# Performance work log

Measured on AMD Instinct MI355X. Metric: run time of the kernel, lower is better.

Reference implementation:

```python
import math
import jax, jax.numpy as jnp
import numpy as np

B, P, L, D = 2, 32, 32, 768
N = P * L
H = 12
HD = D // H
FF = 4 * D
NL = 12
NC = 1000
EPS = 1e-5
NEG = -jnp.finfo(jnp.float32).max


def sinusoidal_pe(P, L, D):
    pe = np.zeros((P, L, D), dtype=np.float32)
    half = D // 2
    div = np.exp(np.arange(0.0, half, 2) * -(math.log(10000.0) / half))  # (half/2,)
    pos_l = np.arange(0.0, L)[:, None]
    pos_n = np.arange(0.0, P)[:, None]
    # faithful to the (buggy) torch builder, which requires P == L
    pe[:, :, 0:half:2] = np.sin(pos_n * div)[None, :, :]
    pe[:, :, 1:half:2] = np.cos(pos_n * div)[None, :, :]
    pe[:, :, half::2] = np.sin(pos_l * div)[:, None, :]
    pe[:, :, half + 1::2] = np.cos(pos_l * div)[:, None, :]
    return pe.reshape(P * L, D)


def layernorm(x, w, b):
    mu = jnp.mean(x, axis=-1, keepdims=True)
    var = jnp.var(x, axis=-1, keepdims=True)
    return (x - mu) * jax.lax.rsqrt(var + EPS) * w + b


def setup_inputs() -> dict:
    key = jax.random.key(0)
    ks = jax.random.split(key, 16)
    tn = lambda k, shp: (0.02 * jax.random.normal(k, shp)).astype(jnp.float32)
    inp = {
        "x": jax.random.normal(ks[0], (B, N, D), dtype=jnp.float32),
        "mask": jax.random.randint(ks[1], (B, N), 0, 2).astype(bool),
        "pe": jnp.asarray(sinusoidal_pe(P, L, D)),
        "ln0_w": jnp.ones((NL, D)), "ln0_b": jnp.zeros((NL, D)),
        "qkv_w": tn(ks[2], (NL, D, 3 * D)),
        "proj_w": tn(ks[3], (NL, D, D)), "proj_b": jnp.zeros((NL, D)),
        "ln1_w": jnp.ones((NL, D)), "ln1_b": jnp.zeros((NL, D)),
        "ff1_w": tn(ks[4], (NL, D, FF)), "ff1_b": jnp.zeros((NL, FF)),
        "ff2_w": tn(ks[5], (NL, FF, D)), "ff2_b": jnp.zeros((NL, D)),
        "norm_w": jnp.ones((D,)), "norm_b": jnp.zeros((D,)),
        "pool_w": tn(ks[6], (D, 1)), "pool_b": jnp.zeros((1,)),
        "fc_w": tn(ks[7], (D, NC)), "fc_b": jnp.zeros((NC,)),
    }
    return inp


def reference(x, mask, pe, ln0_w, ln0_b, qkv_w, proj_w, proj_b, ln1_w, ln1_b,
              ff1_w, ff1_b, ff2_w, ff2_b, norm_w, norm_b, pool_w, pool_b, fc_w, fc_b):
    scale = HD ** -0.5
    mask2 = mask[:, None, :] & mask[:, :, None]  # (B,N,N)

    def blk(h, p):
        g0w, g0b, qw, pw, pb, g1w, g1b, f1w, f1b, f2w, f2b = p
        y = layernorm(h, g0w, g0b)
        qkv = (y @ qw).reshape(B, N, 3, H, HD).transpose(2, 0, 3, 1, 4)  # (3,B,H,N,hd)
        q, k, v = qkv[0], qkv[1], qkv[2]
        attn = jnp.einsum('bhnd,bhmd->bhnm', q, k) * scale
        attn = jnp.where(mask2[:, None, :, :], attn, NEG)
        attn = jax.nn.softmax(attn, axis=-1)
        o = jnp.einsum('bhnm,bhmd->bhnd', attn, v)
        o = o.transpose(0, 2, 1, 3).reshape(B, N, D) @ pw + pb
        h = layernorm(h + o, g1w, g1b)
        ff = jax.nn.gelu(h @ f1w + f1b, approximate=False) @ f2w + f2b
        return h + ff, None

    h = x + pe[None]
    params = (ln0_w, ln0_b, qkv_w, proj_w, proj_b, ln1_w, ln1_b, ff1_w, ff1_b, ff2_w, ff2_b)
    h, _ = jax.lax.scan(blk, h, params)
    h = layernorm(h, norm_w, norm_b)
    # seq-pool: softmax over tokens of a learned scalar score
    w = jax.nn.softmax(h @ pool_w + pool_b, axis=1)  # (B,N,1)
    pooled = jnp.einsum('bnc,bnd->bd', w, h)  # c == 1
    return pooled @ fc_w + fc_b
```

## Files before the change

kernel.cpp:

```cpp
#include <hip/hip_runtime.h>
#include <hip/hip_bf16.h>
#include <cfloat>
#include <cmath>

typedef __bf16 bf16x8 __attribute__((ext_vector_type(8)));
typedef __bf16 bf16x4 __attribute__((ext_vector_type(4)));
typedef float  f32x4  __attribute__((ext_vector_type(4)));

static constexpr int Bb = 2, Nn = 1024, Dd = 768, Hh = 12, HDd = 64, FFf = 3072, NLl = 12, NCc = 1000;
static constexpr int Mm = Bb * Nn;
static constexpr float NEGF = -3.402823466e38f;

__device__ __forceinline__ float block_reduce_sum(float v, volatile float* smem) {
  for (int o = 32; o; o >>= 1) v += __shfl_down(v, o);
  int lane = threadIdx.x & 63, w = threadIdx.x >> 6;
  __syncthreads();
  if (lane == 0) smem[w] = v;
  __syncthreads();
  return smem[0] + smem[1] + smem[2] + smem[3];
}

__device__ __forceinline__ float block_reduce_max(float v, volatile float* smem) {
  for (int o = 32; o; o >>= 1) v = fmaxf(v, __shfl_down(v, o));
  int lane = threadIdx.x & 63, w = threadIdx.x >> 6;
  __syncthreads();
  if (lane == 0) smem[w] = v;
  __syncthreads();
  return fmaxf(fmaxf(smem[0], smem[1]), fmaxf(smem[2], smem[3]));
}

__global__ void detect_mask(const unsigned char* __restrict__ m, int* __restrict__ flag) {
  __shared__ int s_nz1, s_nz2, s_nz3, s_nz84, s_pv;
  int tid = threadIdx.x;
  if (tid == 0) { s_nz1 = 0; s_nz2 = 0; s_nz3 = 0; s_nz84 = 0; s_pv = 0; }
  __syncthreads();
  int nz1 = 0, nz2 = 0, nz3 = 0, nz84 = 0, pv = 0;
  for (int i = tid; i < 2048; i += 256) {
    unsigned char v = m[i];
    if (v) {
      int p4 = i & 3;
      if (p4 == 1) nz1 = 1;
      if (p4 == 2) nz2 = 1;
      if (p4 == 3) nz3 = 1;
      if ((i & 7) == 4) nz84 = 1;
      if ((i & 1) == 0) { if (v != 0x80) pv = 1; }
      else              { if (v != 0x3f) pv = 1; }
    }
  }
  if (nz1)  atomicOr(&s_nz1, 1);
  if (nz2)  atomicOr(&s_nz2, 1);
  if (nz3)  atomicOr(&s_nz3, 1);
  if (nz84) atomicOr(&s_nz84, 1);
  if (pv)   atomicOr(&s_pv, 1);
  __syncthreads();
  if (tid == 0) {
    int f;
    if (!s_nz1 && !s_nz2 && !s_nz3) f = s_nz84 ? 0 : 3;
    else if (!s_pv)                 f = s_nz1 ? 4 : 2;
    else                            f = 1;
    *flag = f;
  }
}

__device__ __forceinline__ bool mask_at(const void* mraw, int flag, int idx) {
  switch (flag) {
    case 0:  return ((const int*)mraw)[idx] != 0;
    case 1:  return ((const unsigned char*)mraw)[idx] != 0;
    case 2:  return ((const float*)mraw)[idx] != 0.f;
    case 3:  return ((const long long*)mraw)[idx] != 0;
    default: return ((const unsigned short*)mraw)[idx] != 0;
  }
}

__device__ __forceinline__ void cvt8_store(const float* __restrict__ s, __bf16* __restrict__ d, int j) {
  float4 f0 = reinterpret_cast<const float4*>(s)[j * 2];
  float4 f1 = reinterpret_cast<const float4*>(s)[j * 2 + 1];
  bf16x8 r;
  r[0] = (__bf16)f0.x; r[1] = (__bf16)f0.y; r[2] = (__bf16)f0.z; r[3] = (__bf16)f0.w;
  r[4] = (__bf16)f1.x; r[5] = (__bf16)f1.y; r[6] = (__bf16)f1.z; r[7] = (__bf16)f1.w;
  reinterpret_cast<bf16x8*>(d)[j] = r;
}

__global__ __launch_bounds__(256) void cvt_w(const float* __restrict__ src, __bf16* __restrict__ dst, int n8) {
  int i = blockIdx.x * 256 + threadIdx.x;
  if (i < n8) cvt8_store(src, dst, i);
}

__global__ __launch_bounds__(256) void cvt_w4(const float* __restrict__ sq, const float* __restrict__ sp,
                                              const float* __restrict__ s1, const float* __restrict__ s2,
                                              __bf16* __restrict__ dq, __bf16* __restrict__ dp,
                                              __bf16* __restrict__ d1, __bf16* __restrict__ d2) {
  const int N0 = Dd * 3 * Dd / 8, N1 = Dd * Dd / 8, N2 = Dd * FFf / 8, N3 = FFf * Dd / 8;
  int i = blockIdx.x * 256 + threadIdx.x;
  if (i < N0)                    cvt8_store(sq, dq, i);
  else if (i < N0 + N1)          cvt8_store(sp, dp, i - N0);
  else if (i < N0 + N1 + N2)     cvt8_store(s1, d1, i - N0 - N1);
  else if (i < N0 + N1 + N2 + N3) cvt8_store(s2, d2, i - N0 - N1 - N2);
}

__global__ __launch_bounds__(256) void add_pe_k(const float* __restrict__ x, const float* __restrict__ pe,
                                                float* __restrict__ h) {
  long i = (long)blockIdx.x * 256 + threadIdx.x;
  long nd = i % ((long)Nn * Dd);
  h[i] = x[i] + pe[nd];
}

template<int OBF>
__global__ __launch_bounds__(256) void ln_kernel(const float* __restrict__ X,
                                                 const float* __restrict__ w, const float* __restrict__ b,
                                                 void* __restrict__ Y) {
  __shared__ float smem[4];
  int row = blockIdx.x, tid = threadIdx.x;
  const float* x = X + (size_t)row * Dd;
  float v[3];
  for (int j = 0; j < 3; ++j) v[j] = x[tid + j * 256];
  float s = v[0] + v[1] + v[2];
  s = block_reduce_sum(s, smem);
  float mean = s * (1.f / 768.f);
  float q = 0.f;
  for (int j = 0; j < 3; ++j) { float d = v[j] - mean; q += d * d; }
  q = block_reduce_sum(q, smem);
  float inv = rsqrtf(q * (1.f / 768.f) + 1e-5f);
  for (int j = 0; j < 3; ++j) {
    int c = tid + j * 256;
    float r = (v[j] - mean) * inv * w[c] + b[c];
    if (OBF) ((__bf16*)Y)[(size_t)row * Dd + c] = (__bf16)r;
    else     ((float*)Y)[(size_t)row * Dd + c] = r;
  }
}

template<int OBF, int HRES>
__global__ __launch_bounds__(256) void res_ln_kernel(float* __restrict__ H,
                                                     const float* __restrict__ P0, const float* __restrict__ P1,
                                                     const float* __restrict__ pb,
                                                     const float* __restrict__ w, const float* __restrict__ b,
                                                     void* __restrict__ Y) {
  __shared__ float smem[4];
  int row = blockIdx.x, tid = threadIdx.x;
  float* x  = H  + (size_t)row * Dd;
  const float* p0 = P0 + (size_t)row * Dd;
  const float* p1 = P1 + (size_t)row * Dd;
  float v[3];
  for (int j = 0; j < 3; ++j) {
    int c = tid + j * 256;
    v[j] = x[c] + (p0[c] + p1[c] + pb[c]);
  }
  float s = v[0] + v[1] + v[2];
  s = block_reduce_sum(s, smem);
  float mean = s * (1.f / 768.f);
  float q = 0.f;
  for (int j = 0; j < 3; ++j) { float d = v[j] - mean; q += d * d; }
  q = block_reduce_sum(q, smem);
  float inv = rsqrtf(q * (1.f / 768.f) + 1e-5f);
  for (int j = 0; j < 3; ++j) {
    int c = tid + j * 256;
    float r = (v[j] - mean) * inv * w[c] + b[c];
    x[c] = HRES ? v[j] : r;
    if (OBF) ((__bf16*)Y)[(size_t)row * Dd + c] = (__bf16)r;
    else     ((float*)Y)[(size_t)row * Dd + c] = r;
  }
}

template<int BN, int EPI, int OBF>
__global__ __launch_bounds__(256) void gemm128(
    const __bf16* __restrict__ Ap, long lda,
    const __bf16* __restrict__ Bp, long ldb,
    const float* __restrict__ bias,
    void* __restrict__ Cp, long ldc,
    int Ksize, long czs)
{
  constexpr int FN = BN / 32;
  constexpr int KB = BN / 8;
  int tid = threadIdx.x;

  int nwg2 = gridDim.x * gridDim.y;
  int bid = blockIdx.y * gridDim.x + blockIdx.x;
  int swz = (bid & 7) * (nwg2 >> 3) + (bid >> 3);
  int bx = swz % gridDim.x, by = swz / gridDim.x;
  int m0 = by * 128, n0 = bx * BN;
  int z = blockIdx.z;

  const __bf16* Aq = Ap + (long)z * Ksize;
  const __bf16* Bq = Bp + (long)z * Ksize * ldb;

  __shared__ __align__(16) __bf16 Ah[128][40];
  __shared__ __align__(16) __bf16 Bh[BN][40];

  f32x4 acc[4][FN];
  #pragma unroll
  for (int i = 0; i < 4; ++i)
    #pragma unroll
    for (int j = 0; j < FN; ++j)
      #pragma unroll
      for (int k = 0; k < 4; ++k) acc[i][j][k] = 0.f;

  int lane = tid & 63;
  int w = tid >> 6;
  int WR = (w >> 1) * 64, WC = (w & 1) * (BN / 2);
  int fr = lane & 15, kg = lane >> 4;

  const int ar = tid >> 1, acs = (tid & 1) * 16;
  const int bn = tid % BN;
  const int kb = (tid / BN) * KB;

  const __bf16* Abase = Aq + (long)(m0 + ar) * lda + acs;
  const __bf16* Bbase = Bq + (long)kb * ldb + (n0 + bn);

  bf16x8 pa0, pa1;
  __bf16 pbh[KB];
  {
    pa0 = *reinterpret_cast<const bf16x8*>(Abase);
    pa1 = *reinterpret_cast<const bf16x8*>(Abase + 8);
    #pragma unroll
    for (int j = 0; j < KB; ++j) pbh[j] = Bbase[(long)j * ldb];
  }

  for (int k0 = 0; k0 < Ksize; k0 += 32) {
    __syncthreads();
    {
      *reinterpret_cast<bf16x8*>(&Ah[ar][acs]) = pa0;
      *reinterpret_cast<bf16x8*>(&Ah[ar][acs + 8]) = pa1;
      #pragma unroll
      for (int g8 = 0; g8 < KB / 8; ++g8)
        *reinterpret_cast<bf16x8*>(&Bh[bn][kb + g8 * 8]) = *reinterpret_cast<bf16x8*>(&pbh[g8 * 8]);
    }
    __syncthreads();

    if (k0 + 32 < Ksize) {
      const __bf16* As = Abase + (k0 + 32);
      pa0 = *reinterpret_cast<const bf16x8*>(As);
      pa1 = *reinterpret_cast<const bf16x8*>(As + 8);
      const __bf16* Bs = Bbase + (long)(k0 + 32) * ldb;
      #pragma unroll
      for (int j = 0; j < KB; ++j) pbh[j] = Bs[(long)j * ldb];
    }

    bf16x8 ah[4], bh[FN];
    #pragma unroll
    for (int fm = 0; fm < 4; ++fm)
      ah[fm] = *reinterpret_cast<const bf16x8*>(&Ah[WR + fm * 16 + fr][kg * 8]);
    #pragma unroll
    for (int fn = 0; fn < FN; ++fn)
      bh[fn] = *reinterpret_cast<const bf16x8*>(&Bh[WC + fn * 16 + fr][kg * 8]);
    #pragma unroll
    for (int fm = 0; fm < 4; ++fm)
      #pragma unroll
      for (int fn = 0; fn < FN; ++fn)
        acc[fm][fn] = __builtin_amdgcn_mfma_f32_16x16x32_bf16(ah[fm], bh[fn], acc[fm][fn], 0, 0, 0);
  }

  #pragma unroll
  for (int fm = 0; fm < 4; ++fm)
    #pragma unroll
    for (int fn = 0; fn < FN; ++fn)
      #pragma unroll
      for (int i = 0; i < 4; ++i) {
        int rowg = m0 + WR + fm * 16 + kg * 4 + i;
        int coln = n0 + WC + fn * 16 + fr;
        float v = acc[fm][fn][i];
        if (EPI >= 1) v += bias[coln];
        if (EPI == 2) v = 0.5f * v * (1.f + erff(v * 0.70710678118654752f));
        long ci = (long)z * czs + (long)rowg * ldc + coln;
        if (OBF) ((__bf16*)Cp)[ci] = (__bf16)v;
        else     ((float*)Cp)[ci] = v;
      }
}

__global__ __launch_bounds__(256) void flash_attn_split(const __bf16* __restrict__ qkvb,
                                                        const void* __restrict__ mraw,
                                                        const int* __restrict__ flagp,
                                                        float* __restrict__ p0, float* __restrict__ p1,
                                                        float2* __restrict__ ml) {
  __shared__ __align__(16) __bf16 Qs[64][72];
  __shared__ __align__(16) __bf16 Ks[64][72];
  __shared__ __align__(16) __bf16 Vt[64][66];
  __shared__ __align__(16) __bf16 Ps[64][72];
  __shared__ float kmf[64];
  __shared__ float qmf[64];

  int s = blockIdx.z & 1, b = blockIdx.z >> 1;
  int hh = blockIdx.y;
  int q0 = blockIdx.x * 64;
  int tid = threadIdx.x, lane = tid & 63, w = tid >> 6;
  int flag = *flagp;
  int fr = lane & 15, kg = lane >> 4;

  const int sr = tid >> 2;
  const int sc = (tid & 3) * 16;

  {
    const __bf16* Qsrc = qkvb + ((long)(b * Nn + q0 + sr)) * (3 * Dd) + hh * HDd + sc;
    *reinterpret_cast<bf16x8*>(&Qs[sr][sc])     = *reinterpret_cast<const bf16x8*>(Qsrc);
    *reinterpret_cast<bf16x8*>(&Qs[sr][sc + 8]) = *reinterpret_cast<const bf16x8*>(Qsrc + 8);
    if (tid < 64) qmf[tid] = mask_at(mraw, flag, b * Nn + q0 + tid) ? 1.f : 0.f;
  }
  __syncthreads();

  float qm[4];
  #pragma unroll
  for (int i = 0; i < 4; ++i) qm[i] = qmf[16 * w + kg * 4 + i];

  bf16x8 qa[2];
  #pragma unroll
  for (int ks = 0; ks < 2; ++ks)
    qa[ks] = *reinterpret_cast<const bf16x8*>(&Qs[16 * w + fr][ks * 32 + kg * 8]);

  float mrow[4], lrow[4];
  f32x4 accO[4];
  #pragma unroll
  for (int i = 0; i < 4; ++i) { mrow[i] = -INFINITY; lrow[i] = 0.f; }
  #pragma unroll
  for (int t = 0; t < 4; ++t)
    for (int i = 0; i < 4; ++i) accO[t][i] = 0.f;

  const int jbeg = s * (Nn / 2), jend = jbeg + (Nn / 2);

  bf16x8 rk0, rk1, rv0, rv1;
  {
    const __bf16* Ksrc = qkvb + ((long)(b * Nn + jbeg + sr)) * (3 * Dd) + Dd + hh * HDd + sc;
    const __bf16* Vsrc = Ksrc + Dd;
    rk0 = *reinterpret_cast<const bf16x8*>(Ksrc);
    rk1 = *reinterpret_cast<const bf16x8*>(Ksrc + 8);
    rv0 = *reinterpret_cast<const bf16x8*>(Vsrc);
    rv1 = *reinterpret_cast<const bf16x8*>(Vsrc + 8);
  }

  for (int j0 = jbeg; j0 < jend; j0 += 64) {
    __syncthreads();
    {
      *reinterpret_cast<bf16x8*>(&Ks[sr][sc])     = rk0;
      *reinterpret_cast<bf16x8*>(&Ks[sr][sc + 8]) = rk1;
      #pragma unroll
      for (int j = 0; j < 8; ++j) {
        Vt[sc + j][sr]     = rv0[j];
        Vt[sc + 8 + j][sr] = rv1[j];
      }
      if (tid < 64) kmf[tid] = mask_at(mraw, flag, b * Nn + j0 + tid) ? 1.f : 0.f;
    }
    __syncthreads();

    if (j0 + 64 < jend) {
      const __bf16* Ksrc = qkvb + ((long)(b * Nn + j0 + 64 + sr)) * (3 * Dd) + Dd + hh * HDd + sc;
      const __bf16* Vsrc = Ksrc + Dd;
      rk0 = *reinterpret_cast<const bf16x8*>(Ksrc);
      rk1 = *reinterpret_cast<const bf16x8*>(Ksrc + 8);
      rv0 = *reinterpret_cast<const bf16x8*>(Vsrc);
      rv1 = *reinterpret_cast<const bf16x8*>(Vsrc + 8);
    }

    f32x4 sacc[4];
    #pragma unroll
    for (int t = 0; t < 4; ++t)
      for (int i = 0; i < 4; ++i) sacc[t][i] = 0.f;
    #pragma unroll
    for (int ks = 0; ks < 2; ++ks) {
      #pragma unroll
      for (int t = 0; t < 4; ++t) {
        bf16x8 bh = *reinterpret_cast<const bf16x8*>(&Ks[16 * t + fr][ks * 32 + kg * 8]);
        sacc[t] = __builtin_amdgcn_mfma_f32_16x16x32_bf16(qa[ks], bh, sacc[t], 0, 0, 0);
      }
    }

    float sv[4][4];
    float mt[4] = {-INFINITY, -INFINITY, -INFINITY, -INFINITY};
    #pragma unroll
    for (int t = 0; t < 4; ++t) {
      float km = kmf[16 * t + fr];
      #pragma unroll
      for (int i = 0; i < 4; ++i) {
        float sx = (km > 0.f && qm[i] > 0.f) ? sacc[t][i] * 0.125f : NEGF;
        sv[t][i] = sx;
        mt[i] = fmaxf(mt[i], sx);
      }
    }
    #pragma unroll
    for (int off = 8; off; off >>= 1)
      #pragma unroll
      for (int i = 0; i < 4; ++i) mt[i] = fmaxf(mt[i], __shfl_xor(mt[i], off));

    float r[4], psum[4];
    #pragma unroll
    for (int i = 0; i < 4; ++i) {
      float mn = fmaxf(mrow[i], mt[i]);
      r[i] = __expf(mrow[i] - mn);
      mrow[i] = mn;
      psum[i] = 0.f;
    }
    #pragma unroll
    for (int t = 0; t < 4; ++t) {
      #pragma unroll
      for (int i = 0; i < 4; ++i) {
        float p = __expf(sv[t][i] - mrow[i]);
        psum[i] += p;
        Ps[16 * w + kg * 4 + i][16 * t + fr] = (__bf16)p;
      }
    }
    #pragma unroll
    for (int off = 8; off; off >>= 1)
      #pragma unroll
      for (int i = 0; i < 4; ++i) psum[i] += __shfl_xor(psum[i], off);
    #pragma unroll
    for (int i = 0; i < 4; ++i) lrow[i] = lrow[i] * r[i] + psum[i];
    #pragma unroll
    for (int t = 0; t < 4; ++t)
      #pragma unroll
      for (int i = 0; i < 4; ++i) accO[t][i] *= r[i];

    __syncthreads();

    #pragma unroll
    for (int ks = 0; ks < 2; ++ks) {
      bf16x8 pa = *reinterpret_cast<const bf16x8*>(&Ps[16 * w + fr][ks * 32 + kg * 8]);
      #pragma unroll
      for (int t2 = 0; t2 < 4; ++t2) {
        bf16x8 vb = *reinterpret_cast<const bf16x8*>(&Vt[16 * t2 + fr][ks * 32 + kg * 8]);
        accO[t2] = __builtin_amdgcn_mfma_f32_16x16x32_bf16(pa, vb, accO[t2], 0, 0, 0);
      }
    }
  }

  float* op = s ? p1 : p0;
  #pragma unroll
  for (int t2 = 0; t2 < 4; ++t2)
    #pragma unroll
    for (int i = 0; i < 4; ++i) {
      int qrow = q0 + 16 * w + kg * 4 + i;
      int col = 16 * t2 + fr;
      op[((long)(b * Nn + qrow)) * Dd + hh * HDd + col] = accO[t2][i];
    }
  if (fr == 0) {
    #pragma unroll
    for (int i = 0; i < 4; ++i) {
      int qrow = q0 + 16 * w + kg * 4 + i;
      ml[((long)(s * Bb + b) * Hh + hh) * Nn + qrow] = make_float2(mrow[i], lrow[i]);
    }
  }
}

__global__ __launch_bounds__(256) void flash_combine(const float* __restrict__ p0, const float* __restrict__ p1,
                                                     const float2* __restrict__ ml, __bf16* __restrict__ ob) {
  long i4 = (long)blockIdx.x * 256 + threadIdx.x;
  long i = i4 * 4;
  int d = (int)(i % Dd);
  long row = i / Dd;
  int b = (int)(row >> 10), n = (int)(row & (Nn - 1));
  int hh = d >> 6;
  float2 a = ml[((long)b * Hh + hh) * Nn + n];
  float2 c = ml[(((long)Bb + b) * Hh + hh) * Nn + n];
  float M = fmaxf(a.x, c.x);
  float w0 = __expf(a.x - M), w1 = __expf(c.x - M);
  float inv = 1.f / (w0 * a.y + w1 * c.y);
  float4 v0 = reinterpret_cast<const float4*>(p0)[i4];
  float4 v1 = reinterpret_cast<const float4*>(p1)[i4];
  bf16x4 r;
  r[0] = (__bf16)((w0 * v0.x + w1 * v1.x) * inv);
  r[1] = (__bf16)((w0 * v0.y + w1 * v1.y) * inv);
  r[2] = (__bf16)((w0 * v0.z + w1 * v1.z) * inv);
  r[3] = (__bf16)((w0 * v0.w + w1 * v1.w) * inv);
  *reinterpret_cast<bf16x4*>(&ob[i]) = r;
}

__global__ __launch_bounds__(256) void pool_score(const float* __restrict__ hn, const float* __restrict__ pw,
                                                  const float* __restrict__ pb, float* __restrict__ s) {
  __shared__ float smem[4];
  int row = blockIdx.x, tid = threadIdx.x;
  const float* x = hn + (size_t)row * Dd;
  float acc = 0.f;
  for (int j = 0; j < 3; ++j) { int c = tid + j * 256; acc += x[c] * pw[c]; }
  acc = block_reduce_sum(acc, smem);
  if (tid == 0) s[row] = acc + pb[0];
}

__global__ __launch_bounds__(256) void pool_softmax(const float* __restrict__ s, float* __restrict__ w) {
  __shared__ float smem[4];
  int b = blockIdx.x, tid = threadIdx.x;
  const float* x = s + b * Nn;
  float v[4];
  for (int j = 0; j < 4; ++j) v[j] = x[tid * 4 + j];
  float mx = fmaxf(fmaxf(v[0], v[1]), fmaxf(v[2], v[3]));
  mx = block_reduce_max(mx, smem);
  float e[4], sum = 0.f;
  for (int j = 0; j < 4; ++j) { e[j] = expf(v[j] - mx); sum += e[j]; }
  sum = block_reduce_sum(sum, smem);
  float inv = 1.f / sum;
  for (int j = 0; j < 4; ++j) w[b * Nn + tid * 4 + j] = e[j] * inv;
}

__global__ __launch_bounds__(256) void pool_reduce1(const float* __restrict__ hn, const float* __restrict__ w,
                                                    float* __restrict__ part) {
  int d = blockIdx.x * 256 + threadIdx.x;
  int ch = blockIdx.y, b = blockIdx.z;
  int n0 = ch * 128;
  float a0 = 0.f, a1 = 0.f;
  for (int n = n0; n < n0 + 128; n += 2) {
    a0 = fmaf(w[b * Nn + n],     hn[((size_t)(b * Nn + n))     * Dd + d], a0);
    a1 = fmaf(w[b * Nn + n + 1], hn[((size_t)(b * Nn + n + 1)) * Dd + d], a1);
  }
  part[((size_t)(b * 8 + ch)) * Dd + d] = a0 + a1;
}

__global__ __launch_bounds__(256) void pool_reduce2(const float* __restrict__ part, float* __restrict__ pooled) {
  int d = blockIdx.x * 256 + threadIdx.x;
  int b = blockIdx.y;
  float s = 0.f;
  #pragma unroll
  for (int ch = 0; ch < 8; ++ch) s += part[((size_t)(b * 8 + ch)) * Dd + d];
  pooled[b * Dd + d] = s;
}

__global__ __launch_bounds__(256) void fc_kernel(const float* __restrict__ pooled, const float* __restrict__ fw,
                                                 const float* __restrict__ fb, float* __restrict__ out) {
  __shared__ float p[768];
  int b = blockIdx.y, tid = threadIdx.x;
  for (int j = 0; j < 3; ++j) p[tid + j * 256] = pooled[b * Dd + tid + j * 256];
  __syncthreads();
  int c = blockIdx.x * 256 + tid;
  if (c < NCc) {
    float a0 = 0.f, a1 = 0.f, a2 = 0.f, a3 = 0.f;
    #pragma unroll 4
    for (int d = 0; d < Dd; d += 4) {
      a0 = fmaf(p[d],     fw[(size_t)d       * NCc + c], a0);
      a1 = fmaf(p[d + 1], fw[(size_t)(d + 1) * NCc + c], a1);
      a2 = fmaf(p[d + 2], fw[(size_t)(d + 2) * NCc + c], a2);
      a3 = fmaf(p[d + 3], fw[(size_t)(d + 3) * NCc + c], a3);
    }
    out[b * NCc + c] = fb[c] + ((a0 + a1) + (a2 + a3));
  }
}

extern "C" void kernel_launch(void* const* d_in, const int* in_sizes, int n_in,
                              void* d_out, int out_size, void* d_ws, size_t ws_size,
                              hipStream_t stream) {
  const float* x      = (const float*)d_in[0];
  const void*  mask   = d_in[1];
  const float* pe     = (const float*)d_in[2];
  const float* ln0_w  = (const float*)d_in[3];
  const float* ln0_b  = (const float*)d_in[4];
  const float* qkv_w  = (const float*)d_in[5];
  const float* proj_w = (const float*)d_in[6];
  const float* proj_b = (const float*)d_in[7];
  const float* ln1_w  = (const float*)d_in[8];
  const float* ln1_b  = (const float*)d_in[9];
  const float* ff1_w  = (const float*)d_in[10];
  const float* ff1_b  = (const float*)d_in[11];
  const float* ff2_w  = (const float*)d_in[12];
  const float* ff2_b  = (const float*)d_in[13];
  const float* norm_w = (const float*)d_in[14];
  const float* norm_b = (const float*)d_in[15];
  const float* pool_w = (const float*)d_in[16];
  const float* pool_b = (const float*)d_in[17];
  const float* fc_w   = (const float*)d_in[18];
  const float* fc_b   = (const float*)d_in[19];
  float* out = (float*)d_out;

  float* ws = (float*)d_ws;
  float*  h     = ws;
  float*  s0    = h + (long)Mm * Dd;
  float*  s1    = s0 + (long)Mm * Dd;
  __bf16* qkvb  = (__bf16*)(s1 + (long)Mm * Dd);
  __bf16* ob    = qkvb + (long)Mm * 3 * Dd;
  __bf16* yb    = ob + (long)Mm * Dd;

  const bool bigws = ws_size >= (size_t)54 * 1024 * 1024;
  __bf16* wreg = yb + (long)Mm * Dd;
  __bf16 *wq, *wp, *w1, *w2;
  __bf16* wend;
  if (bigws) {
    wq = wreg;
    wp = wq + (long)Dd * 3 * Dd;
    w1 = wp + (long)Dd * Dd;
    w2 = w1 + (long)Dd * FFf;
    wend = w2 + (long)FFf * Dd;
  } else {
    wq = wp = w1 = w2 = wreg;
    wend = wreg + (long)Dd * FFf;
  }
  float*  tail  = (float*)wend;
  float*  spool  = tail;
  float*  wpool  = spool + Mm;
  float*  pooled = wpool + Mm;
  float*  ppart  = pooled + Bb * Dd;
  float*  mlbuf  = ppart + (long)Bb * 8 * Dd;
  int*    mflag  = (int*)(mlbuf + (long)2 * 2 * Bb * Hh * Nn);
  __bf16* gb = qkvb;
  float*  hn = s0;

  const int n8_qkv  = Dd * 3 * Dd / 8;
  const int n8_proj = Dd * Dd / 8;
  const int n8_ff   = Dd * FFf / 8;
  const int n8_all  = n8_qkv + n8_proj + 2 * n8_ff;

  detect_mask<<<1, 256, 0, stream>>>((const unsigned char*)mask, mflag);
  add_pe_k<<<(Mm * Dd) / 256, 256, 0, stream>>>(x, pe, h);
  ln_kernel<1><<<Mm, 256, 0, stream>>>(h, ln0_w, ln0_b, yb);

  for (int l = 0; l < NLl; ++l) {
    if (bigws) {
      cvt_w4<<<(n8_all + 255) / 256, 256, 0, stream>>>(
          qkv_w + (long)l * Dd * 3 * Dd, proj_w + (long)l * Dd * Dd,
          ff1_w + (long)l * Dd * FFf, ff2_w + (long)l * FFf * Dd,
          wq, wp, w1, w2);
    } else {
      cvt_w<<<(n8_qkv + 255) / 256, 256, 0, stream>>>(qkv_w + (long)l * Dd * 3 * Dd, wq, n8_qkv);
    }

    gemm128<64,0,1><<<dim3(3 * Dd / 64, Mm / 128, 1), 256, 0, stream>>>(
        yb, Dd, wq, 3 * Dd, nullptr, qkvb, 3 * Dd, Dd, 0);

    flash_attn_split<<<dim3(Nn / 64, Hh, Bb * 2), 256, 0, stream>>>(
        qkvb, mask, mflag, s0, s1, (float2*)mlbuf);
    flash_combine<<<(Mm * Dd / 4) / 256, 256, 0, stream>>>(s0, s1, (const float2*)mlbuf, ob);

    if (!bigws)
      cvt_w<<<(n8_proj + 255) / 256, 256, 0, stream>>>(proj_w + (long)l * Dd * Dd, wp, n8_proj);
    gemm128<64,0,0><<<dim3(Dd / 64, Mm / 128, 2), 256, 0, stream>>>(
        ob, Dd, wp, Dd, nullptr, s0, Dd, Dd / 2, (long)(s1 - s0));

    res_ln_kernel<1,0><<<Mm, 256, 0, stream>>>(h, s0, s1, proj_b + l * Dd,
                                               ln1_w + l * Dd, ln1_b + l * Dd, yb);

    if (!bigws)
      cvt_w<<<(n8_ff + 255) / 256, 256, 0, stream>>>(ff1_w + (long)l * Dd * FFf, w1, n8_ff);
    gemm128<64,2,1><<<dim3(FFf / 64, Mm / 128, 1), 256, 0, stream>>>(
        yb, Dd, w1, FFf, ff1_b + l * FFf, gb, FFf, Dd, 0);

    if (!bigws)
      cvt_w<<<(n8_ff + 255) / 256, 256, 0, stream>>>(ff2_w + (long)l * FFf * Dd, w2, n8_ff);
    gemm128<64,0,0><<<dim3(Dd / 64, Mm / 128, 2), 256, 0, stream>>>(
        gb, FFf, w2, Dd, nullptr, s0, Dd, FFf / 2, (long)(s1 - s0));

    if (l + 1 < NLl) {
      res_ln_kernel<1,1><<<Mm, 256, 0, stream>>>(h, s0, s1, ff2_b + l * Dd,
                                                 ln0_w + (l + 1) * Dd, ln0_b + (l + 1) * Dd, yb);
    } else {
      res_ln_kernel<0,1><<<Mm, 256, 0, stream>>>(h, s0, s1, ff2_b + l * Dd,
                                                 norm_w, norm_b, hn);
    }
  }

  pool_score<<<Mm, 256, 0, stream>>>(hn, pool_w, pool_b, spool);
  pool_softmax<<<Bb, 256, 0, stream>>>(spool, wpool);
  pool_reduce1<<<dim3(Dd / 256, 8, Bb), 256, 0, stream>>>(hn, wpool, ppart);
  pool_reduce2<<<dim3(Dd / 256, Bb), 256, 0, stream>>>(ppart, pooled);
  fc_kernel<<<dim3(4, Bb), 256, 0, stream>>>(pooled, fc_w, fc_b, out);
}
```

Before: 1.966 ms.

## Fuse flash-attention split combine into projection GEMM A-tile load

Removes the separate flash_combine kernel and has a new projection GEMM variant read the two fp32 partial attention outputs and the (max, sum) statistics directly. It merges them and converts to bf16 while staging the A tile into shared memory. The GEMM output now goes into the qkv buffer region, reused as fp32 scratch, so the attention partials in s0/s1 stay intact. This saves one kernel launch and the bf16 write and read of the combined output. In exchange, the GEMM loads twice as many fp32 bytes per A element, and the two z-splits each redo the combine for their K half.

```diff
diff --git a/kernel.cpp b/kernel.cpp
--- a/kernel.cpp
+++ b/kernel.cpp
@@ -266,6 +266,136 @@
       }
 }
 
+template<int BN>
+__global__ __launch_bounds__(256) void gemm128_pc(
+    const float* __restrict__ S0, const float* __restrict__ S1,
+    const float2* __restrict__ Ml,
+    const __bf16* __restrict__ Bp, long ldb,
+    float* __restrict__ Cp, long ldc,
+    int Ksize, long czs)
+{
+  constexpr int FN = BN / 32;
+  constexpr int KB = BN / 8;
+  int tid = threadIdx.x;
+
+  int nwg2 = gridDim.x * gridDim.y;
+  int bid = blockIdx.y * gridDim.x + blockIdx.x;
+  int swz = (bid & 7) * (nwg2 >> 3) + (bid >> 3);
+  int bx = swz % gridDim.x, by = swz / gridDim.x;
+  int m0 = by * 128, n0 = bx * BN;
+  int z = blockIdx.z;
+
+  const __bf16* Bq = Bp + (long)z * Ksize * ldb;
+
+  __shared__ __align__(16) __bf16 Ah[128][40];
+  __shared__ __align__(16) __bf16 Bh[BN][40];
+
+  f32x4 acc[4][FN];
+  #pragma unroll
+  for (int i = 0; i < 4; ++i)
+    #pragma unroll
+    for (int j = 0; j < FN; ++j)
+      #pragma unroll
+      for (int k = 0; k < 4; ++k) acc[i][j][k] = 0.f;
+
+  int lane = tid & 63;
+  int w = tid >> 6;
+  int WR = (w >> 1) * 64, WC = (w & 1) * (BN / 2);
+  int fr = lane & 15, kg = lane >> 4;
+
+  const int ar = tid >> 1, acs = (tid & 1) * 16;
+  const int bn = tid % BN;
+  const int kb = (tid / BN) * KB;
+
+  const int r = m0 + ar;
+  const int bidx = r >> 10, nrow = r & (Nn - 1);
+  const float* S0r = S0 + (long)r * Dd;
+  const float* S1r = S1 + (long)r * Dd;
+  const __bf16* Bbase = Bq + (long)kb * ldb + (n0 + bn);
+
+  float ps0[16], ps1[16];
+  float2 mlA, mlC;
+  __bf16 pbh[KB];
+  {
+    int col = z * Ksize + acs;
+    *reinterpret_cast<float4*>(&ps0[0])  = *reinterpret_cast<const float4*>(S0r + col);
+    *reinterpret_cast<float4*>(&ps0[4])  = *reinterpret_cast<const float4*>(S0r + col + 4);
+    *reinterpret_cast<float4*>(&ps0[8])  = *reinterpret_cast<const float4*>(S0r + col + 8);
+    *reinterpret_cast<float4*>(&ps0[12]) = *reinterpret_cast<const float4*>(S0r + col + 12);
+    *reinterpret_cast<float4*>(&ps1[0])  = *reinterpret_cast<const float4*>(S1r + col);
+    *reinterpret_cast<float4*>(&ps1[4])  = *reinterpret_cast<const float4*>(S1r + col + 4);
+    *reinterpret_cast<float4*>(&ps1[8])  = *reinterpret_cast<const float4*>(S1r + col + 8);
+    *reinterpret_cast<float4*>(&ps1[12]) = *reinterpret_cast<const float4*>(S1r + col + 12);
+    int hh = col >> 6;
+    mlA = Ml[((long)bidx * Hh + hh) * Nn + nrow];
+    mlC = Ml[(((long)Bb + bidx) * Hh + hh) * Nn + nrow];
+    #pragma unroll
+    for (int j = 0; j < KB; ++j) pbh[j] = Bbase[(long)j * ldb];
+  }
+
+  for (int k0 = 0; k0 < Ksize; k0 += 32) {
+    __syncthreads();
+    {
+      float M = fmaxf(mlA.x, mlC.x);
+      float w0 = __expf(mlA.x - M), w1 = __expf(mlC.x - M);
+      float inv = 1.f / (w0 * mlA.y + w1 * mlC.y);
+      bf16x8 t0, t1;
+      #pragma unroll
+      for (int j = 0; j < 8; ++j) t0[j] = (__bf16)((w0 * ps0[j] + w1 * ps1[j]) * inv);
+      #pragma unroll
+      for (int j = 0; j < 8; ++j) t1[j] = (__bf16)((w0 * ps0[8 + j] + w1 * ps1[8 + j]) * inv);
+      *reinterpret_cast<bf16x8*>(&Ah[ar][acs]) = t0;
+      *reinterpret_cast<bf16x8*>(&Ah[ar][acs + 8]) = t1;
+      #pragma unroll
+      for (int g8 = 0; g8 < KB / 8; ++g8)
+        *reinterpret_cast<bf16x8*>(&Bh[bn][kb + g8 * 8]) = *reinterpret_cast<bf16x8*>(&pbh[g8 * 8]);
+    }
+    __syncthreads();
+
+    if (k0 + 32 < Ksize) {
+      int col = z * Ksize + k0 + 32 + acs;
+      *reinterpret_cast<float4*>(&ps0[0])  = *reinterpret_cast<const float4*>(S0r + col);
+      *reinterpret_cast<float4*>(&ps0[4])  = *reinterpret_cast<const float4*>(S0r + col + 4);
+      *reinterpret_cast<float4*>(&ps0[8])  = *reinterpret_cast<const float4*>(S0r + col + 8);
+      *reinterpret_cast<float4*>(&ps0[12]) = *reinterpret_cast<const float4*>(S0r + col + 12);
+      *reinterpret_cast<float4*>(&ps1[0])  = *reinterpret_cast<const float4*>(S1r + col);
+      *reinterpret_cast<float4*>(&ps1[4])  = *reinterpret_cast<const float4*>(S1r + col + 4);
+      *reinterpret_cast<float4*>(&ps1[8])  = *reinterpret_cast<const float4*>(S1r + col + 8);
+      *reinterpret_cast<float4*>(&ps1[12]) = *reinterpret_cast<const float4*>(S1r + col + 12);
+      int hh = col >> 6;
+      mlA = Ml[((long)bidx * Hh + hh) * Nn + nrow];
+      mlC = Ml[(((long)Bb + bidx) * Hh + hh) * Nn + nrow];
+      const __bf16* Bs = Bbase + (long)(k0 + 32) * ldb;
+      #pragma unroll
+      for (int j = 0; j < KB; ++j) pbh[j] = Bs[(long)j * ldb];
+    }
+
+    bf16x8 ah[4], bh[FN];
+    #pragma unroll
+    for (int fm = 0; fm < 4; ++fm)
+      ah[fm] = *reinterpret_cast<const bf16x8*>(&Ah[WR + fm * 16 + fr][kg * 8]);
+    #pragma unroll
+    for (int fn = 0; fn < FN; ++fn)
+      bh[fn] = *reinterpret_cast<const bf16x8*>(&Bh[WC + fn * 16 + fr][kg * 8]);
+    #pragma unroll
+    for (int fm = 0; fm < 4; ++fm)
+      #pragma unroll
+      for (int fn = 0; fn < FN; ++fn)
+        acc[fm][fn] = __builtin_amdgcn_mfma_f32_16x16x32_bf16(ah[fm], bh[fn], acc[fm][fn], 0, 0, 0);
+  }
+
+  #pragma unroll
+  for (int fm = 0; fm < 4; ++fm)
+    #pragma unroll
+    for (int fn = 0; fn < FN; ++fn)
+      #pragma unroll
+      for (int i = 0; i < 4; ++i) {
+        int rowg = m0 + WR + fm * 16 + kg * 4 + i;
+        int coln = n0 + WC + fn * 16 + fr;
+        Cp[(long)z * czs + (long)rowg * ldc + coln] = acc[fm][fn][i];
+      }
+}
+
 __global__ __launch_bounds__(256) void flash_attn_split(const __bf16* __restrict__ qkvb,
                                                         const void* __restrict__ mraw,
                                                         const int* __restrict__ flagp,
@@ -435,29 +565,6 @@
       ml[((long)(s * Bb + b) * Hh + hh) * Nn + qrow] = make_float2(mrow[i], lrow[i]);
     }
   }
-}
-
-__global__ __launch_bounds__(256) void flash_combine(const float* __restrict__ p0, const float* __restrict__ p1,
-                                                     const float2* __restrict__ ml, __bf16* __restrict__ ob) {
-  long i4 = (long)blockIdx.x * 256 + threadIdx.x;
-  long i = i4 * 4;
-  int d = (int)(i % Dd);
-  long row = i / Dd;
-  int b = (int)(row >> 10), n = (int)(row & (Nn - 1));
-  int hh = d >> 6;
-  float2 a = ml[((long)b * Hh + hh) * Nn + n];
-  float2 c = ml[(((long)Bb + b) * Hh + hh) * Nn + n];
-  float M = fmaxf(a.x, c.x);
-  float w0 = __expf(a.x - M), w1 = __expf(c.x - M);
-  float inv = 1.f / (w0 * a.y + w1 * c.y);
-  float4 v0 = reinterpret_cast<const float4*>(p0)[i4];
-  float4 v1 = reinterpret_cast<const float4*>(p1)[i4];
-  bf16x4 r;
-  r[0] = (__bf16)((w0 * v0.x + w1 * v1.x) * inv);
-  r[1] = (__bf16)((w0 * v0.y + w1 * v1.y) * inv);
-  r[2] = (__bf16)((w0 * v0.z + w1 * v1.z) * inv);
-  r[3] = (__bf16)((w0 * v0.w + w1 * v1.w) * inv);
-  *reinterpret_cast<bf16x4*>(&ob[i]) = r;
 }
 
 __global__ __launch_bounds__(256) void pool_score(const float* __restrict__ hn, const float* __restrict__ pw,
@@ -561,6 +668,9 @@
   __bf16* ob    = qkvb + (long)Mm * 3 * Dd;
   __bf16* yb    = ob + (long)Mm * Dd;
 
+  float* pp0 = (float*)qkvb;
+  float* pp1 = pp0 + (long)Mm * Dd;
+
   const bool bigws = ws_size >= (size_t)54 * 1024 * 1024;
   __bf16* wreg = yb + (long)Mm * Dd;
   __bf16 *wq, *wp, *w1, *w2;
@@ -609,14 +719,13 @@
 
     flash_attn_split<<<dim3(Nn / 64, Hh, Bb * 2), 256, 0, stream>>>(
         qkvb, mask, mflag, s0, s1, (float2*)mlbuf);
-    flash_combine<<<(Mm * Dd / 4) / 256, 256, 0, stream>>>(s0, s1, (const float2*)mlbuf, ob);
 
     if (!bigws)
       cvt_w<<<(n8_proj + 255) / 256, 256, 0, stream>>>(proj_w + (long)l * Dd * Dd, wp, n8_proj);
-    gemm128<64,0,0><<<dim3(Dd / 64, Mm / 128, 2), 256, 0, stream>>>(
-        ob, Dd, wp, Dd, nullptr, s0, Dd, Dd / 2, (long)(s1 - s0));
-
-    res_ln_kernel<1,0><<<Mm, 256, 0, stream>>>(h, s0, s1, proj_b + l * Dd,
+    gemm128_pc<64><<<dim3(Dd / 64, Mm / 128, 2), 256, 0, stream>>>(
+        s0, s1, (const float2*)mlbuf, wp, Dd, pp0, Dd, Dd / 2, (long)(pp1 - pp0));
+
+    res_ln_kernel<1,0><<<Mm, 256, 0, stream>>>(h, pp0, pp1, proj_b + l * Dd,
                                                ln1_w + l * Dd, ln1_b + l * Dd, yb);
 
     if (!bigws)
```

Result: no change. 1.975 ms (+0.4%).
